# Kernel optimization log

Measured on AMD Instinct MI355X. Metric: run time of the kernel, lower is better.

The kernel has to match this reference:

```python
import jax, jax.numpy as jnp
import numpy as np

B, T, E, H, N_TAGS = 128, 512, 256, 512, 32
START, END = 30, 31


def setup_inputs() -> dict:
    key = jax.random.key(0)
    ks = jax.random.split(key, 12)
    s = 1.0 / np.sqrt(H)

    def w(k, shape):
        return jax.random.normal(k, shape, jnp.float32) * s

    X = jax.random.normal(ks[0], (B, T, E), jnp.float32)
    length = jnp.sort(jax.random.randint(ks[1], (B,), T // 2, T + 1))[::-1]
    masks = (jnp.arange(T)[None, :] < length[:, None]).astype(jnp.float32)
    W_ih_f, W_hh_f, b_f = w(ks[2], (4 * H, E)), w(ks[3], (4 * H, H)), w(ks[4], (4 * H,))
    W_ih_b, W_hh_b, b_b = w(ks[5], (4 * H, E)), w(ks[6], (4 * H, H)), w(ks[7], (4 * H,))
    W_out, b_out = w(ks[8], (N_TAGS, 2 * H)), w(ks[9], (N_TAGS,))
    transitions = jax.random.normal(ks[10], (N_TAGS, N_TAGS), jnp.float32)
    transitions = transitions.at[:, START].set(-1e4).at[END, :].set(-1e4)
    return dict(X=X, masks=masks, length=length,
                W_ih_f=W_ih_f, W_hh_f=W_hh_f, b_f=b_f,
                W_ih_b=W_ih_b, W_hh_b=W_hh_b, b_b=b_b,
                W_out=W_out, b_out=b_out, transitions=transitions)


def _lstm_dir(Xt, mt, Wih, Whh, b, reverse):
    # Xt: [T,B,E], mt: [T,B,1]. Masked update emulates pack_padded_sequence
    # (state frozen on pad; for reverse dir, state stays zero until last valid token).
    h0 = jnp.zeros((Xt.shape[1], H), Xt.dtype)

    def step(carry, inp):
        h, c = carry
        x, m = inp
        gates = x @ Wih.T + h @ Whh.T + b  # [B,4H], torch gate order i,f,g,o
        i, f, g, o = jnp.split(gates, 4, axis=-1)
        i, f, o = jax.nn.sigmoid(i), jax.nn.sigmoid(f), jax.nn.sigmoid(o)
        g = jnp.tanh(g)
        c_new = f * c + i * g
        h_new = o * jnp.tanh(c_new)
        h = m * h_new + (1.0 - m) * h
        c = m * c_new + (1.0 - m) * c
        return (h, c), h

    _, hs = jax.lax.scan(step, (h0, h0), (Xt, mt), reverse=reverse)
    return hs  # [T,B,H]


def reference(X, masks, length, W_ih_f, W_hh_f, b_f, W_ih_b, W_hh_b, b_b, W_out, b_out, transitions):
    Xt = X.transpose(1, 0, 2)            # [T,B,E]
    mT = masks.T                          # [T,B]
    mt = mT[:, :, None]
    hf = _lstm_dir(Xt, mt, W_ih_f, W_hh_f, b_f, False)
    hb = _lstm_dir(Xt, mt, W_ih_b, W_hh_b, b_b, True)
    emis = jnp.concatenate([hf, hb], axis=-1) @ W_out.T + b_out  # [T,B,n_tags]

    # Viterbi forward recurrence with masking
    alphas0 = emis[0] + transitions[START]  # [B,n]

    def vstep(alphas, inp):
        e, m = inp  # e: [B,n], m: [B,1]
        scores = alphas[:, :, None] + transitions[None] + e[:, None, :]  # [B,from,to]
        alphas = m * scores.max(axis=1) + (1.0 - m) * alphas
        return alphas, jnp.argmax(scores, axis=1)

    alphas, bps = jax.lax.scan(vstep, alphas0, (emis[1:], mt[1:]))
    final = alphas + transitions[:, END]
    max_end_scores = final.max(axis=1)      # [B]
    end_tags = jnp.argmax(final, axis=1)    # [B]

    # Masked backtrace: bps[k] is the backpointer into position k+1
    def bstep(cur, inp):
        bp, m = inp  # bp: [B,n], m: [B]
        prev = jnp.where(m > 0, jnp.take_along_axis(bp, cur[:, None], axis=1)[:, 0], cur)
        return prev, prev

    _, outs = jax.lax.scan(bstep, end_tags, (bps, mT[1:]), reverse=True)  # outs[k]=tag at pos k
    tags = jnp.concatenate([outs, end_tags[None]], axis=0).T              # [B,T]
    tags = jnp.where(masks > 0, tags, -1)
    return max_end_scores, tags
```

## Files before the change

kernel.cpp:

```cpp
#include <hip/hip_runtime.h>
#include <cfloat>
#include <cmath>

#define Bn 128
#define Tn 512
#define En 256
#define Hn 512
#define NTAGS 32
#define CHK 64
#define NCHK 12

#define OFF_HF 0
#define OFF_HB 131072
#define OFF_CF 262144
#define OFF_CB 327680
#define OFF_EF 393216
#define OFF_EB 2490368

__device__ __forceinline__ void gll16(const float* g, float* l) {
  __builtin_amdgcn_global_load_lds(
      (const __attribute__((address_space(1))) void*)g,
      (__attribute__((address_space(3))) void*)l, 16, 0, 0);
}

__global__ __launch_bounds__(512, 2) void lstm_step_k(
    const float* __restrict__ X, const float* __restrict__ masks,
    const float* __restrict__ Wih_f, const float* __restrict__ Whh_f, const float* __restrict__ bias_f,
    const float* __restrict__ Wih_b, const float* __restrict__ Whh_b, const float* __restrict__ bias_b,
    const float* __restrict__ Wout, float* __restrict__ ws, int s)
{
  __shared__ __align__(16) float WT[768 * 16];
  __shared__ __align__(16) float HX[2][CHK * Bn];
  __shared__ __align__(16) float GL[Bn * 17];
  __shared__ __align__(16) float WoL[512];
  __shared__ __align__(16) float RS[8 * Bn];

  const int tid  = threadIdx.x;
  const int blk  = blockIdx.x;
  const int lane = tid & 63;
  const int wid  = __builtin_amdgcn_readfirstlane(tid >> 6);
  const int bq   = tid & 15;
  const int cg   = (tid >> 4) & 1;
  const int ks   = tid >> 5;

  const int dir = blk >> 7;
  const int bbk = blk & 127;
  const int t = dir ? (Tn - 1 - s) : s;
  const float* Wih  = dir ? Wih_b  : Wih_f;
  const float* Whh  = dir ? Whh_b  : Whh_f;
  const float* bias = dir ? bias_b : bias_f;
  float* hbuf = ws + (dir ? OFF_HB : OFF_HF);
  float* cbuf = ws + (dir ? OFF_CB : OFF_CF);
  const int rbuf = (s + 1) & 1;
  const int wbuf = s & 1;
  const float* hprev = hbuf + rbuf * (Hn * Bn);
  float*       hnext = hbuf + wbuf * (Hn * Bn);
  const int hidx0 = bbk * 4;

  const int etag = bbk & 31;
  const int ebq  = bbk >> 5;

  #pragma unroll
  for (int r = 0; r < 4; ++r) {
    const int item = r * 512 + tid;
    gll16(hprev + item * 4, &HX[0][item * 4]);
  }
  {
    const int lc = tid & 15;
    const int kw = tid >> 4;
    const int row = (lc >> 2) * Hn + hidx0 + (lc & 3);
    #pragma unroll
    for (int i = 0; i < 6; ++i) {
      const int k = (kw + i * 32) * 4;
      float4 w4;
      if (k < Hn) w4 = *(const float4*)&Whh[(size_t)row * Hn + k];
      else        w4 = *(const float4*)&Wih[(size_t)row * En + (k - Hn)];
      WT[(k + 0) * 16 + lc] = w4.x; WT[(k + 1) * 16 + lc] = w4.y;
      WT[(k + 2) * 16 + lc] = w4.z; WT[(k + 3) * 16 + lc] = w4.w;
    }
  }
  if (tid < 128) {
    const float4 wo = *(const float4*)&Wout[(size_t)etag * (2 * Hn) + dir * Hn + tid * 4];
    *(float4*)&WoL[tid * 4] = wo;
  }
  __syncthreads();

  float acc[8][8];
  #pragma unroll
  for (int m = 0; m < 8; ++m)
    #pragma unroll
    for (int n = 0; n < 8; ++n) acc[m][n] = 0.f;
  float eac[8] = {0.f, 0.f, 0.f, 0.f, 0.f, 0.f, 0.f, 0.f};

  const int xbq = tid & 127;
  const int xeg = tid >> 7;

  #pragma unroll 1
  for (int c = 0; c < NCHK; ++c) {
    const int nxt = c + 1;
    float4 st[4];
    if (nxt < 8) {
      const float* src = hprev + nxt * (CHK * Bn);
      float* dst = &HX[nxt & 1][0];
      #pragma unroll
      for (int r = 0; r < 4; ++r) {
        const int item = r * 512 + tid;
        gll16(src + item * 4, dst + item * 4);
      }
    } else if (nxt < NCHK) {
      const int e0 = (nxt - 8) * CHK;
      #pragma unroll
      for (int r = 0; r < 4; ++r)
        st[r] = *(const float4*)&X[(size_t)xbq * (Tn * En) + (size_t)t * En + e0 + xeg * 16 + r * 4];
    }

    {
      const float* HXc = &HX[c & 1][0];
      #pragma unroll
      for (int j = 0; j < 4; ++j) {
        const int kl = ks * 4 + j;
        const int kg = c * 64 + kl;
        const float4 a0 = *(const float4*)&HXc[kl * Bn + bq * 4];
        const float4 a1 = *(const float4*)&HXc[kl * Bn + 64 + bq * 4];
        const float4 w0 = *(const float4*)&WT[kg * 16 + cg * 8];
        const float4 w1 = *(const float4*)&WT[kg * 16 + cg * 8 + 4];
        const float a_[8] = {a0.x, a0.y, a0.z, a0.w, a1.x, a1.y, a1.z, a1.w};
        const float w_[8] = {w0.x, w0.y, w0.z, w0.w, w1.x, w1.y, w1.z, w1.w};
        #pragma unroll
        for (int m = 0; m < 8; ++m)
          #pragma unroll
          for (int n = 0; n < 8; ++n)
            acc[m][n] += a_[m] * w_[n];
        if (c < 8) {
          const float wo = WoL[kg];
          #pragma unroll
          for (int m = 0; m < 8; ++m) eac[m] += a_[m] * wo;
        }
      }
    }

    if (nxt >= 8 && nxt < NCHK) {
      float* dst = &HX[nxt & 1][0];
      #pragma unroll
      for (int r = 0; r < 4; ++r) {
        const int el = xeg * 16 + r * 4;
        dst[(el + 0) * Bn + xbq] = st[r].x;
        dst[(el + 1) * Bn + xbq] = st[r].y;
        dst[(el + 2) * Bn + xbq] = st[r].z;
        dst[(el + 3) * Bn + xbq] = st[r].w;
      }
    }
    __syncthreads();
  }

  #pragma unroll
  for (int m = 0; m < 8; ++m)
    #pragma unroll
    for (int n = 0; n < 8; ++n)
      acc[m][n] += __shfl_xor(acc[m][n], 32);
  #pragma unroll
  for (int m = 0; m < 8; ++m) eac[m] += __shfl_xor(eac[m], 32);

  float* P = &HX[0][0];
  if ((lane >> 5) == 0) {
    #pragma unroll
    for (int n = 0; n < 8; ++n) {
      *(float4*)&P[wid * 2048 + (cg * 8 + n) * Bn + bq * 4] =
          make_float4(acc[0][n], acc[1][n], acc[2][n], acc[3][n]);
      *(float4*)&P[wid * 2048 + (cg * 8 + n) * Bn + 64 + bq * 4] =
          make_float4(acc[4][n], acc[5][n], acc[6][n], acc[7][n]);
    }
    if (cg == 0) {
      *(float4*)&RS[wid * Bn + bq * 4] = make_float4(eac[0], eac[1], eac[2], eac[3]);
      *(float4*)&RS[wid * Bn + 64 + bq * 4] = make_float4(eac[4], eac[5], eac[6], eac[7]);
    }
  }
  __syncthreads();
  {
    const int b  = tid & 127;
    const int cq = tid >> 7;
    #pragma unroll
    for (int nn = 0; nn < 4; ++nn) {
      const int n = cq * 4 + nn;
      float v = 0.f;
      #pragma unroll
      for (int k2 = 0; k2 < 8; ++k2)
        v += P[k2 * 2048 + n * Bn + b];
      GL[b * 17 + n] = v;
    }
  }
  if (s > 0 && ebq == 0 && tid < 128) {
    const int tprev = dir ? (Tn - s) : (s - 1);
    float* Edst = ws + (dir ? OFF_EB : OFF_EF);
    float v = 0.f;
    #pragma unroll
    for (int g = 0; g < 8; ++g) v += RS[g * Bn + tid];
    Edst[(size_t)tprev * (NTAGS * Bn) + etag * Bn + tid] = v;
  }
  __syncthreads();

  {
    const int b  = tid & 127;
    const int hh = tid >> 7;
    const int hidx = hidx0 + hh;
    const float gi = GL[b * 17 + hh]      + bias[hidx];
    const float gf = GL[b * 17 + 4 + hh]  + bias[Hn + hidx];
    const float gc = GL[b * 17 + 8 + hh]  + bias[2 * Hn + hidx];
    const float go = GL[b * 17 + 12 + hh] + bias[3 * Hn + hidx];
    const float iv = 1.f / (1.f + expf(-gi));
    const float fv = 1.f / (1.f + expf(-gf));
    const float gv = tanhf(gc);
    const float ov = 1.f / (1.f + expf(-go));
    const float cold = cbuf[hidx * Bn + b];
    const float cnew = fv * cold + iv * gv;
    const float hold = hprev[hidx * Bn + b];
    const float hnew = ov * tanhf(cnew);
    const float m = masks[(size_t)b * Tn + t];
    hnext[hidx * Bn + b] = (m > 0.f) ? hnew : hold;
    cbuf[hidx * Bn + b]  = (m > 0.f) ? cnew : cold;
  }
}

__global__ __launch_bounds__(512) void emis_final_k(const float* __restrict__ Wout,
                                                    float* __restrict__ ws)
{
  __shared__ float RSf[16 * Bn];
  const int tid = threadIdx.x;
  const int dir = blockIdx.x >> 5;
  const int tag = blockIdx.x & 31;
  const float* hsrc = ws + (dir ? OFF_HB : OFF_HF) + 1 * (Hn * Bn);
  const int tprev = dir ? 0 : (Tn - 1);
  const float* wrow = Wout + (size_t)tag * (2 * Hn) + dir * Hn;
  float* Edst = ws + (dir ? OFF_EB : OFF_EF);
  const int bq = tid & 31;
  const int kg = tid >> 5;
  float4 a4 = make_float4(0.f, 0.f, 0.f, 0.f);
  #pragma unroll 4
  for (int kk = 0; kk < 32; ++kk) {
    const int k = kg * 32 + kk;
    const float w = wrow[k];
    const float4 h4 = *(const float4*)&hsrc[k * Bn + bq * 4];
    a4.x += h4.x * w; a4.y += h4.y * w; a4.z += h4.z * w; a4.w += h4.w * w;
  }
  *(float4*)&RSf[kg * Bn + bq * 4] = a4;
  __syncthreads();
  if (tid < 128) {
    float v = 0.f;
    #pragma unroll
    for (int g = 0; g < 16; ++g) v += RSf[g * Bn + tid];
    Edst[(size_t)tprev * (NTAGS * Bn) + tag * Bn + tid] = v;
  }
}

__global__ __launch_bounds__(64) void viterbi_k(
    const float* __restrict__ Ef, const float* __restrict__ Eb,
    const float* __restrict__ bout, const float* __restrict__ trans,
    const float* __restrict__ masks, float* __restrict__ out)
{
  const int b = blockIdx.x;
  const int l = threadIdx.x;
  __shared__ float tr[32][32];
  __shared__ float al[32];
  __shared__ float msk[512];
  __shared__ unsigned char bp[512][32];
  __shared__ int tseq[512];

  for (int i = l; i < 1024; i += 64) tr[i >> 5][i & 31] = trans[i];
  for (int i = l; i < 512; i += 64) msk[i] = masks[(size_t)b * 512 + i];
  __syncthreads();

  const int j  = l & 31;
  const int hi = l >> 5;
  if (l < 32)
    al[j] = Ef[(size_t)j * Bn + b] + Eb[(size_t)j * Bn + b] + bout[j] + tr[30][j];
  __syncthreads();

  for (int t = 1; t < 512; ++t) {
    float pmax = -FLT_MAX; int pidx = 0;
    #pragma unroll
    for (int ii = 0; ii < 16; ++ii) {
      const int i = hi * 16 + ii;
      const float sc = al[i] + tr[i][j];
      if (sc > pmax) { pmax = sc; pidx = i; }
    }
    const float omax = __shfl_down(pmax, 32);
    const int   oidx = __shfl_down(pidx, 32);
    if (l < 32) {
      if (omax > pmax) { pmax = omax; pidx = oidx; }
      bp[t][j] = (unsigned char)pidx;
      const float e = Ef[(size_t)t * (NTAGS * Bn) + j * Bn + b]
                    + Eb[(size_t)t * (NTAGS * Bn) + j * Bn + b] + bout[j];
      const float na = pmax + e;
      if (msk[t] > 0.f) al[j] = na;
    }
    __syncthreads();
  }

  float fv; int fidx;
  if (l < 32) { fv = al[l] + tr[l][31]; fidx = l; }
  else        { fv = -FLT_MAX; fidx = 1 << 30; }
  #pragma unroll
  for (int off = 16; off >= 1; off >>= 1) {
    const float v2 = __shfl_xor(fv, off);
    const int   i2 = __shfl_xor(fidx, off);
    if (v2 > fv || (v2 == fv && i2 < fidx)) { fv = v2; fidx = i2; }
  }
  if (l == 0) {
    out[b] = fv;
    int cur = fidx;
    tseq[511] = cur;
    for (int t = 511; t >= 1; --t) {
      const int prev = (msk[t] > 0.f) ? (int)bp[t][cur] : cur;
      tseq[t - 1] = prev;
      cur = prev;
    }
  }
  __syncthreads();
  for (int t = l; t < 512; t += 64) {
    const float tv = (msk[t] > 0.f) ? (float)tseq[t] : -1.0f;
    out[Bn + (size_t)b * 512 + t] = tv;
  }
}

extern "C" void kernel_launch(void* const* d_in, const int* in_sizes, int n_in,
                              void* d_out, int out_size, void* d_ws, size_t ws_size,
                              hipStream_t stream) {
  const float* X      = (const float*)d_in[0];
  const float* masks  = (const float*)d_in[1];
  const float* Wih_f  = (const float*)d_in[3];
  const float* Whh_f  = (const float*)d_in[4];
  const float* bf     = (const float*)d_in[5];
  const float* Wih_b  = (const float*)d_in[6];
  const float* Whh_b  = (const float*)d_in[7];
  const float* bb     = (const float*)d_in[8];
  const float* Wout   = (const float*)d_in[9];
  const float* bout   = (const float*)d_in[10];
  const float* trans  = (const float*)d_in[11];
  float* ws  = (float*)d_ws;
  float* out = (float*)d_out;

  hipMemsetAsync(d_ws, 0, (size_t)OFF_EF * sizeof(float), stream);

  for (int s = 0; s < Tn; ++s)
    lstm_step_k<<<256, 512, 0, stream>>>(X, masks, Wih_f, Whh_f, bf,
                                         Wih_b, Whh_b, bb, Wout, ws, s);
  emis_final_k<<<64, 512, 0, stream>>>(Wout, ws);
  viterbi_k<<<128, 64, 0, stream>>>(ws + OFF_EF, ws + OFF_EB, bout, trans, masks, out);
}
```

Before: 12.22 ms.

## Fuse per-timestep LSTM launches into one persistent kernel with grid barrier

Replaces 512 separate step-kernel launches with a single persistent kernel that loops over timesteps. Blocks synchronize through a two-level atomic grid barrier. The recurrent weights stay resident in LDS instead of being reloaded every step, and cell state and the own-h value stay in registers, which removes the c buffer from global memory. The aim is to cut launch overhead and repeated weight staging. The risks are deadlock if all 256 blocks are not co-resident, and the timeout guard in the barrier, which could silently break correctness.

```diff
diff --git a/kernel.cpp b/kernel.cpp
--- a/kernel.cpp
+++ b/kernel.cpp
@@ -12,10 +12,9 @@
 
 #define OFF_HF 0
 #define OFF_HB 131072
-#define OFF_CF 262144
-#define OFF_CB 327680
-#define OFF_EF 393216
-#define OFF_EB 2490368
+#define OFF_BAR 262144
+#define OFF_EF 263168
+#define OFF_EB (OFF_EF + Tn * NTAGS * Bn)
 
 __device__ __forceinline__ void gll16(const float* g, float* l) {
   __builtin_amdgcn_global_load_lds(
@@ -23,11 +22,44 @@
       (__attribute__((address_space(3))) void*)l, 16, 0, 0);
 }
 
-__global__ __launch_bounds__(512, 2) void lstm_step_k(
+__device__ __forceinline__ void gridbar(unsigned* bar, int blk, int tid, unsigned target) {
+  __syncthreads();
+  if (tid == 0) {
+    __threadfence();
+    unsigned* root_phase = bar;
+    unsigned* root_cnt   = bar + 32;
+    const int g = blk >> 4;
+    unsigned* gcnt   = bar + 64  + g * 32;
+    unsigned* gphase = bar + 640 + g * 32;
+    unsigned o = __hip_atomic_fetch_add(gcnt, 1u, __ATOMIC_ACQ_REL, __HIP_MEMORY_SCOPE_AGENT);
+    if (o == 15u) {
+      __hip_atomic_store(gcnt, 0u, __ATOMIC_RELAXED, __HIP_MEMORY_SCOPE_AGENT);
+      unsigned r = __hip_atomic_fetch_add(root_cnt, 1u, __ATOMIC_ACQ_REL, __HIP_MEMORY_SCOPE_AGENT);
+      if (r == 15u) {
+        __hip_atomic_store(root_cnt, 0u, __ATOMIC_RELAXED, __HIP_MEMORY_SCOPE_AGENT);
+        __hip_atomic_store(root_phase, target, __ATOMIC_RELEASE, __HIP_MEMORY_SCOPE_AGENT);
+      } else {
+        int guard = 0;
+        while (__hip_atomic_load(root_phase, __ATOMIC_RELAXED, __HIP_MEMORY_SCOPE_AGENT) < target
+               && ++guard < 50000) __builtin_amdgcn_s_sleep(16);
+        (void)__hip_atomic_load(root_phase, __ATOMIC_ACQUIRE, __HIP_MEMORY_SCOPE_AGENT);
+      }
+      __hip_atomic_store(gphase, target, __ATOMIC_RELEASE, __HIP_MEMORY_SCOPE_AGENT);
+    } else {
+      int guard = 0;
+      while (__hip_atomic_load(gphase, __ATOMIC_RELAXED, __HIP_MEMORY_SCOPE_AGENT) < target
+             && ++guard < 50000) __builtin_amdgcn_s_sleep(16);
+      (void)__hip_atomic_load(gphase, __ATOMIC_ACQUIRE, __HIP_MEMORY_SCOPE_AGENT);
+    }
+  }
+  __syncthreads();
+}
+
+__global__ __launch_bounds__(512, 2) void lstm_persist_k(
     const float* __restrict__ X, const float* __restrict__ masks,
     const float* __restrict__ Wih_f, const float* __restrict__ Whh_f, const float* __restrict__ bias_f,
     const float* __restrict__ Wih_b, const float* __restrict__ Whh_b, const float* __restrict__ bias_b,
-    const float* __restrict__ Wout, float* __restrict__ ws, int s)
+    const float* __restrict__ Wout, float* __restrict__ ws)
 {
   __shared__ __align__(16) float WT[768 * 16];
   __shared__ __align__(16) float HX[2][CHK * Bn];
@@ -45,26 +77,16 @@
 
   const int dir = blk >> 7;
   const int bbk = blk & 127;
-  const int t = dir ? (Tn - 1 - s) : s;
   const float* Wih  = dir ? Wih_b  : Wih_f;
   const float* Whh  = dir ? Whh_b  : Whh_f;
   const float* bias = dir ? bias_b : bias_f;
   float* hbuf = ws + (dir ? OFF_HB : OFF_HF);
-  float* cbuf = ws + (dir ? OFF_CB : OFF_CF);
-  const int rbuf = (s + 1) & 1;
-  const int wbuf = s & 1;
-  const float* hprev = hbuf + rbuf * (Hn * Bn);
-  float*       hnext = hbuf + wbuf * (Hn * Bn);
+  float* Edst = ws + (dir ? OFF_EB : OFF_EF);
+  unsigned* bar = (unsigned*)(ws + OFF_BAR);
   const int hidx0 = bbk * 4;
-
   const int etag = bbk & 31;
   const int ebq  = bbk >> 5;
 
-  #pragma unroll
-  for (int r = 0; r < 4; ++r) {
-    const int item = r * 512 + tid;
-    gll16(hprev + item * 4, &HX[0][item * 4]);
-  }
   {
     const int lc = tid & 15;
     const int kw = tid >> 4;
@@ -83,141 +105,160 @@
     const float4 wo = *(const float4*)&Wout[(size_t)etag * (2 * Hn) + dir * Hn + tid * 4];
     *(float4*)&WoL[tid * 4] = wo;
   }
-  __syncthreads();
-
-  float acc[8][8];
-  #pragma unroll
-  for (int m = 0; m < 8; ++m)
-    #pragma unroll
-    for (int n = 0; n < 8; ++n) acc[m][n] = 0.f;
-  float eac[8] = {0.f, 0.f, 0.f, 0.f, 0.f, 0.f, 0.f, 0.f};
+
+  const int pb  = tid & 127;
+  const int phh = tid >> 7;
+  const int hidxp = hidx0 + phh;
+  const float bi  = bias[hidxp];
+  const float bf_ = bias[Hn + hidxp];
+  const float bg_ = bias[2 * Hn + hidxp];
+  const float bo_ = bias[3 * Hn + hidxp];
+  float h_reg = 0.f, c_reg = 0.f;
 
   const int xbq = tid & 127;
   const int xeg = tid >> 7;
+  __syncthreads();
 
   #pragma unroll 1
-  for (int c = 0; c < NCHK; ++c) {
-    const int nxt = c + 1;
-    float4 st[4];
-    if (nxt < 8) {
-      const float* src = hprev + nxt * (CHK * Bn);
-      float* dst = &HX[nxt & 1][0];
-      #pragma unroll
-      for (int r = 0; r < 4; ++r) {
-        const int item = r * 512 + tid;
-        gll16(src + item * 4, dst + item * 4);
-      }
-    } else if (nxt < NCHK) {
-      const int e0 = (nxt - 8) * CHK;
-      #pragma unroll
-      for (int r = 0; r < 4; ++r)
-        st[r] = *(const float4*)&X[(size_t)xbq * (Tn * En) + (size_t)t * En + e0 + xeg * 16 + r * 4];
-    }
-
+  for (int s = 0; s < Tn; ++s) {
+    const int t = dir ? (Tn - 1 - s) : s;
+    const float* hprev = hbuf + ((s + 1) & 1) * (Hn * Bn);
+    float*       hnext = hbuf + (s & 1) * (Hn * Bn);
+    const float mval = masks[(size_t)pb * Tn + t];
+
+    #pragma unroll
+    for (int r = 0; r < 4; ++r) {
+      const int item = r * 512 + tid;
+      gll16(hprev + item * 4, &HX[0][item * 4]);
+    }
+    __syncthreads();
+
+    float acc[8][8];
+    #pragma unroll
+    for (int m = 0; m < 8; ++m)
+      #pragma unroll
+      for (int n = 0; n < 8; ++n) acc[m][n] = 0.f;
+    float eac[8] = {0.f, 0.f, 0.f, 0.f, 0.f, 0.f, 0.f, 0.f};
+
+    #pragma unroll 1
+    for (int c = 0; c < NCHK; ++c) {
+      const int nxt = c + 1;
+      float4 st[4];
+      if (nxt < 8) {
+        const float* src = hprev + nxt * (CHK * Bn);
+        float* dst = &HX[nxt & 1][0];
+        #pragma unroll
+        for (int r = 0; r < 4; ++r) {
+          const int item = r * 512 + tid;
+          gll16(src + item * 4, dst + item * 4);
+        }
+      } else if (nxt < NCHK) {
+        const int e0 = (nxt - 8) * CHK;
+        #pragma unroll
+        for (int r = 0; r < 4; ++r)
+          st[r] = *(const float4*)&X[(size_t)xbq * (Tn * En) + (size_t)t * En + e0 + xeg * 16 + r * 4];
+      }
+
+      {
+        const float* HXc = &HX[c & 1][0];
+        #pragma unroll
+        for (int j = 0; j < 4; ++j) {
+          const int kl = ks * 4 + j;
+          const int kg = c * 64 + kl;
+          const float4 a0 = *(const float4*)&HXc[kl * Bn + bq * 4];
+          const float4 a1 = *(const float4*)&HXc[kl * Bn + 64 + bq * 4];
+          const float4 w0 = *(const float4*)&WT[kg * 16 + cg * 8];
+          const float4 w1 = *(const float4*)&WT[kg * 16 + cg * 8 + 4];
+          const float a_[8] = {a0.x, a0.y, a0.z, a0.w, a1.x, a1.y, a1.z, a1.w};
+          const float w_[8] = {w0.x, w0.y, w0.z, w0.w, w1.x, w1.y, w1.z, w1.w};
+          #pragma unroll
+          for (int m = 0; m < 8; ++m)
+            #pragma unroll
+            for (int n = 0; n < 8; ++n)
+              acc[m][n] += a_[m] * w_[n];
+          if (c < 8) {
+            const float wo = WoL[kg];
+            #pragma unroll
+            for (int m = 0; m < 8; ++m) eac[m] += a_[m] * wo;
+          }
+        }
+      }
+
+      if (nxt >= 8 && nxt < NCHK) {
+        float* dst = &HX[nxt & 1][0];
+        #pragma unroll
+        for (int r = 0; r < 4; ++r) {
+          const int el = xeg * 16 + r * 4;
+          dst[(el + 0) * Bn + xbq] = st[r].x;
+          dst[(el + 1) * Bn + xbq] = st[r].y;
+          dst[(el + 2) * Bn + xbq] = st[r].z;
+          dst[(el + 3) * Bn + xbq] = st[r].w;
+        }
+      }
+      __syncthreads();
+    }
+
+    #pragma unroll
+    for (int m = 0; m < 8; ++m)
+      #pragma unroll
+      for (int n = 0; n < 8; ++n)
+        acc[m][n] += __shfl_xor(acc[m][n], 32);
+    #pragma unroll
+    for (int m = 0; m < 8; ++m) eac[m] += __shfl_xor(eac[m], 32);
+
+    float* P = &HX[0][0];
+    if ((lane >> 5) == 0) {
+      #pragma unroll
+      for (int n = 0; n < 8; ++n) {
+        *(float4*)&P[wid * 2048 + (cg * 8 + n) * Bn + bq * 4] =
+            make_float4(acc[0][n], acc[1][n], acc[2][n], acc[3][n]);
+        *(float4*)&P[wid * 2048 + (cg * 8 + n) * Bn + 64 + bq * 4] =
+            make_float4(acc[4][n], acc[5][n], acc[6][n], acc[7][n]);
+      }
+      if (cg == 0) {
+        *(float4*)&RS[wid * Bn + bq * 4] = make_float4(eac[0], eac[1], eac[2], eac[3]);
+        *(float4*)&RS[wid * Bn + 64 + bq * 4] = make_float4(eac[4], eac[5], eac[6], eac[7]);
+      }
+    }
+    __syncthreads();
     {
-      const float* HXc = &HX[c & 1][0];
-      #pragma unroll
-      for (int j = 0; j < 4; ++j) {
-        const int kl = ks * 4 + j;
-        const int kg = c * 64 + kl;
-        const float4 a0 = *(const float4*)&HXc[kl * Bn + bq * 4];
-        const float4 a1 = *(const float4*)&HXc[kl * Bn + 64 + bq * 4];
-        const float4 w0 = *(const float4*)&WT[kg * 16 + cg * 8];
-        const float4 w1 = *(const float4*)&WT[kg * 16 + cg * 8 + 4];
-        const float a_[8] = {a0.x, a0.y, a0.z, a0.w, a1.x, a1.y, a1.z, a1.w};
-        const float w_[8] = {w0.x, w0.y, w0.z, w0.w, w1.x, w1.y, w1.z, w1.w};
-        #pragma unroll
-        for (int m = 0; m < 8; ++m)
-          #pragma unroll
-          for (int n = 0; n < 8; ++n)
-            acc[m][n] += a_[m] * w_[n];
-        if (c < 8) {
-          const float wo = WoL[kg];
-          #pragma unroll
-          for (int m = 0; m < 8; ++m) eac[m] += a_[m] * wo;
-        }
-      }
-    }
-
-    if (nxt >= 8 && nxt < NCHK) {
-      float* dst = &HX[nxt & 1][0];
-      #pragma unroll
-      for (int r = 0; r < 4; ++r) {
-        const int el = xeg * 16 + r * 4;
-        dst[(el + 0) * Bn + xbq] = st[r].x;
-        dst[(el + 1) * Bn + xbq] = st[r].y;
-        dst[(el + 2) * Bn + xbq] = st[r].z;
-        dst[(el + 3) * Bn + xbq] = st[r].w;
-      }
+      const int b  = tid & 127;
+      const int cq = tid >> 7;
+      #pragma unroll
+      for (int nn = 0; nn < 4; ++nn) {
+        const int n = cq * 4 + nn;
+        float v = 0.f;
+        #pragma unroll
+        for (int k2 = 0; k2 < 8; ++k2)
+          v += P[k2 * 2048 + n * Bn + b];
+        GL[b * 17 + n] = v;
+      }
+    }
+    if (s > 0 && ebq == 0 && tid < 128) {
+      const int tprev = dir ? (Tn - s) : (s - 1);
+      float v = 0.f;
+      #pragma unroll
+      for (int g = 0; g < 8; ++g) v += RS[g * Bn + tid];
+      Edst[(size_t)tprev * (NTAGS * Bn) + etag * Bn + tid] = v;
     }
     __syncthreads();
-  }
-
-  #pragma unroll
-  for (int m = 0; m < 8; ++m)
-    #pragma unroll
-    for (int n = 0; n < 8; ++n)
-      acc[m][n] += __shfl_xor(acc[m][n], 32);
-  #pragma unroll
-  for (int m = 0; m < 8; ++m) eac[m] += __shfl_xor(eac[m], 32);
-
-  float* P = &HX[0][0];
-  if ((lane >> 5) == 0) {
-    #pragma unroll
-    for (int n = 0; n < 8; ++n) {
-      *(float4*)&P[wid * 2048 + (cg * 8 + n) * Bn + bq * 4] =
-          make_float4(acc[0][n], acc[1][n], acc[2][n], acc[3][n]);
-      *(float4*)&P[wid * 2048 + (cg * 8 + n) * Bn + 64 + bq * 4] =
-          make_float4(acc[4][n], acc[5][n], acc[6][n], acc[7][n]);
-    }
-    if (cg == 0) {
-      *(float4*)&RS[wid * Bn + bq * 4] = make_float4(eac[0], eac[1], eac[2], eac[3]);
-      *(float4*)&RS[wid * Bn + 64 + bq * 4] = make_float4(eac[4], eac[5], eac[6], eac[7]);
-    }
-  }
-  __syncthreads();
-  {
-    const int b  = tid & 127;
-    const int cq = tid >> 7;
-    #pragma unroll
-    for (int nn = 0; nn < 4; ++nn) {
-      const int n = cq * 4 + nn;
-      float v = 0.f;
-      #pragma unroll
-      for (int k2 = 0; k2 < 8; ++k2)
-        v += P[k2 * 2048 + n * Bn + b];
-      GL[b * 17 + n] = v;
-    }
-  }
-  if (s > 0 && ebq == 0 && tid < 128) {
-    const int tprev = dir ? (Tn - s) : (s - 1);
-    float* Edst = ws + (dir ? OFF_EB : OFF_EF);
-    float v = 0.f;
-    #pragma unroll
-    for (int g = 0; g < 8; ++g) v += RS[g * Bn + tid];
-    Edst[(size_t)tprev * (NTAGS * Bn) + etag * Bn + tid] = v;
-  }
-  __syncthreads();
-
-  {
-    const int b  = tid & 127;
-    const int hh = tid >> 7;
-    const int hidx = hidx0 + hh;
-    const float gi = GL[b * 17 + hh]      + bias[hidx];
-    const float gf = GL[b * 17 + 4 + hh]  + bias[Hn + hidx];
-    const float gc = GL[b * 17 + 8 + hh]  + bias[2 * Hn + hidx];
-    const float go = GL[b * 17 + 12 + hh] + bias[3 * Hn + hidx];
-    const float iv = 1.f / (1.f + expf(-gi));
-    const float fv = 1.f / (1.f + expf(-gf));
-    const float gv = tanhf(gc);
-    const float ov = 1.f / (1.f + expf(-go));
-    const float cold = cbuf[hidx * Bn + b];
-    const float cnew = fv * cold + iv * gv;
-    const float hold = hprev[hidx * Bn + b];
-    const float hnew = ov * tanhf(cnew);
-    const float m = masks[(size_t)b * Tn + t];
-    hnext[hidx * Bn + b] = (m > 0.f) ? hnew : hold;
-    cbuf[hidx * Bn + b]  = (m > 0.f) ? cnew : cold;
+
+    {
+      const float gi = GL[pb * 17 + phh]       + bi;
+      const float gf = GL[pb * 17 + 4 + phh]   + bf_;
+      const float gc = GL[pb * 17 + 8 + phh]   + bg_;
+      const float go = GL[pb * 17 + 12 + phh]  + bo_;
+      const float iv = 1.f / (1.f + expf(-gi));
+      const float fv = 1.f / (1.f + expf(-gf));
+      const float gv = tanhf(gc);
+      const float ov = 1.f / (1.f + expf(-go));
+      const float cnew = fv * c_reg + iv * gv;
+      const float hnew = ov * tanhf(cnew);
+      if (mval > 0.f) { h_reg = hnew; c_reg = cnew; }
+      hnext[hidxp * Bn + pb] = h_reg;
+    }
+
+    gridbar(bar, blk, tid, (unsigned)(s + 1));
   }
 }
 
@@ -341,9 +382,8 @@
 
   hipMemsetAsync(d_ws, 0, (size_t)OFF_EF * sizeof(float), stream);
 
-  for (int s = 0; s < Tn; ++s)
-    lstm_step_k<<<256, 512, 0, stream>>>(X, masks, Wih_f, Whh_f, bf,
-                                         Wih_b, Whh_b, bb, Wout, ws, s);
+  lstm_persist_k<<<256, 512, 0, stream>>>(X, masks, Wih_f, Whh_f, bf,
+                                          Wih_b, Whh_b, bb, Wout, ws);
   emis_final_k<<<64, 512, 0, stream>>>(Wout, ws);
   viterbi_k<<<128, 64, 0, stream>>>(ws + OFF_EF, ws + OFF_EB, bout, trans, masks, out);
 }
```

New measurement: 18.92 ms. +54.9%, slower.

## Read h and X operands directly from global memory instead of LDS staging

Applied to the files above, without the earlier changes.

Removes the double-buffered LDS staging of the previous hidden state (async global_load_lds) and of the transposed X chunks. Each thread now loads its h and X operands straight from global memory (through cache) inside the GEMM loop, which drops the 12 per-chunk block barriers and shrinks LDS use. The cost is more redundant global/L2 traffic, since several threads read the same activations, and higher load latency with no explicit prefetch. X reads are strided per batch row, so they are less coalesced.

```diff
diff --git a/kernel.cpp b/kernel.cpp
--- a/kernel.cpp
+++ b/kernel.cpp
@@ -7,8 +7,6 @@
 #define En 256
 #define Hn 512
 #define NTAGS 32
-#define CHK 64
-#define NCHK 12
 
 #define OFF_HF 0
 #define OFF_HB 131072
@@ -16,12 +14,6 @@
 #define OFF_CB 327680
 #define OFF_EF 393216
 #define OFF_EB 2490368
-
-__device__ __forceinline__ void gll16(const float* g, float* l) {
-  __builtin_amdgcn_global_load_lds(
-      (const __attribute__((address_space(1))) void*)g,
-      (__attribute__((address_space(3))) void*)l, 16, 0, 0);
-}
 
 __global__ __launch_bounds__(512, 2) void lstm_step_k(
     const float* __restrict__ X, const float* __restrict__ masks,
@@ -30,7 +22,7 @@
     const float* __restrict__ Wout, float* __restrict__ ws, int s)
 {
   __shared__ __align__(16) float WT[768 * 16];
-  __shared__ __align__(16) float HX[2][CHK * Bn];
+  __shared__ __align__(16) float P[8 * 16 * 128];
   __shared__ __align__(16) float GL[Bn * 17];
   __shared__ __align__(16) float WoL[512];
   __shared__ __align__(16) float RS[8 * Bn];
@@ -60,11 +52,6 @@
   const int etag = bbk & 31;
   const int ebq  = bbk >> 5;
 
-  #pragma unroll
-  for (int r = 0; r < 4; ++r) {
-    const int item = r * 512 + tid;
-    gll16(hprev + item * 4, &HX[0][item * 4]);
-  }
   {
     const int lc = tid & 15;
     const int kw = tid >> 4;
@@ -92,65 +79,54 @@
     for (int n = 0; n < 8; ++n) acc[m][n] = 0.f;
   float eac[8] = {0.f, 0.f, 0.f, 0.f, 0.f, 0.f, 0.f, 0.f};
 
-  const int xbq = tid & 127;
-  const int xeg = tid >> 7;
+  #pragma unroll 2
+  for (int c = 0; c < 8; ++c) {
+    #pragma unroll
+    for (int j = 0; j < 4; ++j) {
+      const int kl = ks * 4 + j;
+      const int kg = c * 64 + kl;
+      const float4 a0 = *(const float4*)&hprev[(size_t)kg * Bn + bq * 4];
+      const float4 a1 = *(const float4*)&hprev[(size_t)kg * Bn + 64 + bq * 4];
+      const float4 w0 = *(const float4*)&WT[kg * 16 + cg * 8];
+      const float4 w1 = *(const float4*)&WT[kg * 16 + cg * 8 + 4];
+      const float a_[8] = {a0.x, a0.y, a0.z, a0.w, a1.x, a1.y, a1.z, a1.w};
+      const float w_[8] = {w0.x, w0.y, w0.z, w0.w, w1.x, w1.y, w1.z, w1.w};
+      #pragma unroll
+      for (int m = 0; m < 8; ++m)
+        #pragma unroll
+        for (int n = 0; n < 8; ++n)
+          acc[m][n] += a_[m] * w_[n];
+      const float wo = WoL[kg];
+      #pragma unroll
+      for (int m = 0; m < 8; ++m) eac[m] += a_[m] * wo;
+    }
+  }
 
   #pragma unroll 1
-  for (int c = 0; c < NCHK; ++c) {
-    const int nxt = c + 1;
-    float4 st[4];
-    if (nxt < 8) {
-      const float* src = hprev + nxt * (CHK * Bn);
-      float* dst = &HX[nxt & 1][0];
+  for (int c = 8; c < 12; ++c) {
+    const int e0 = (c - 8) * 64 + ks * 4;
+    float4 xv[8];
+    #pragma unroll
+    for (int m = 0; m < 8; ++m) {
+      const int b = (m < 4) ? (bq * 4 + m) : (64 + bq * 4 + (m - 4));
+      xv[m] = *(const float4*)&X[(size_t)b * (Tn * En) + (size_t)t * En + e0];
+    }
+    #pragma unroll
+    for (int j = 0; j < 4; ++j) {
+      const int kg = c * 64 + ks * 4 + j;
+      const float4 w0 = *(const float4*)&WT[kg * 16 + cg * 8];
+      const float4 w1 = *(const float4*)&WT[kg * 16 + cg * 8 + 4];
+      const float w_[8] = {w0.x, w0.y, w0.z, w0.w, w1.x, w1.y, w1.z, w1.w};
+      const float a_[8] = {((const float*)&xv[0])[j], ((const float*)&xv[1])[j],
+                           ((const float*)&xv[2])[j], ((const float*)&xv[3])[j],
+                           ((const float*)&xv[4])[j], ((const float*)&xv[5])[j],
+                           ((const float*)&xv[6])[j], ((const float*)&xv[7])[j]};
       #pragma unroll
-      for (int r = 0; r < 4; ++r) {
-        const int item = r * 512 + tid;
-        gll16(src + item * 4, dst + item * 4);
-      }
-    } else if (nxt < NCHK) {
-      const int e0 = (nxt - 8) * CHK;
-      #pragma unroll
-      for (int r = 0; r < 4; ++r)
-        st[r] = *(const float4*)&X[(size_t)xbq * (Tn * En) + (size_t)t * En + e0 + xeg * 16 + r * 4];
-    }
-
-    {
-      const float* HXc = &HX[c & 1][0];
-      #pragma unroll
-      for (int j = 0; j < 4; ++j) {
-        const int kl = ks * 4 + j;
-        const int kg = c * 64 + kl;
-        const float4 a0 = *(const float4*)&HXc[kl * Bn + bq * 4];
-        const float4 a1 = *(const float4*)&HXc[kl * Bn + 64 + bq * 4];
-        const float4 w0 = *(const float4*)&WT[kg * 16 + cg * 8];
-        const float4 w1 = *(const float4*)&WT[kg * 16 + cg * 8 + 4];
-        const float a_[8] = {a0.x, a0.y, a0.z, a0.w, a1.x, a1.y, a1.z, a1.w};
-        const float w_[8] = {w0.x, w0.y, w0.z, w0.w, w1.x, w1.y, w1.z, w1.w};
+      for (int m = 0; m < 8; ++m)
         #pragma unroll
-        for (int m = 0; m < 8; ++m)
-          #pragma unroll
-          for (int n = 0; n < 8; ++n)
-            acc[m][n] += a_[m] * w_[n];
-        if (c < 8) {
-          const float wo = WoL[kg];
-          #pragma unroll
-          for (int m = 0; m < 8; ++m) eac[m] += a_[m] * wo;
-        }
-      }
-    }
-
-    if (nxt >= 8 && nxt < NCHK) {
-      float* dst = &HX[nxt & 1][0];
-      #pragma unroll
-      for (int r = 0; r < 4; ++r) {
-        const int el = xeg * 16 + r * 4;
-        dst[(el + 0) * Bn + xbq] = st[r].x;
-        dst[(el + 1) * Bn + xbq] = st[r].y;
-        dst[(el + 2) * Bn + xbq] = st[r].z;
-        dst[(el + 3) * Bn + xbq] = st[r].w;
-      }
-    }
-    __syncthreads();
+        for (int n = 0; n < 8; ++n)
+          acc[m][n] += a_[m] * w_[n];
+    }
   }
 
   #pragma unroll
@@ -161,7 +137,6 @@
   #pragma unroll
   for (int m = 0; m < 8; ++m) eac[m] += __shfl_xor(eac[m], 32);
 
-  float* P = &HX[0][0];
   if ((lane >> 5) == 0) {
     #pragma unroll
     for (int n = 0; n < 8; ++n) {
```

Result: faster. 11.34 ms (-7.2%).
